# Kernel tuning notes

Hardware: AMD Instinct MI355X
Metric: run time of the kernel (lower is better)

Reference implementation:

```python
import jax, jax.numpy as jnp
import jax.lax as lax
import numpy as np

B, T, IN, H, OUT = 1024, 730, 64, 512, 1

def setup_inputs() -> dict:
    key = jax.random.key(0)
    ks = jax.random.split(key, 7)
    s_ih = 1.0 / np.sqrt(IN)
    s_hh = 1.0 / np.sqrt(H)
    return {
        "xd": jax.random.normal(ks[0], (B, T, IN), dtype=jnp.float32),
        "W_ih": jax.random.uniform(ks[1], (4 * H, IN), minval=-s_ih, maxval=s_ih, dtype=jnp.float32),
        "W_hh": jax.random.uniform(ks[2], (4 * H, H), minval=-s_hh, maxval=s_hh, dtype=jnp.float32),
        "b": jax.random.uniform(ks[3], (4 * H,), minval=-s_hh, maxval=s_hh, dtype=jnp.float32),
        "Wl": jax.random.uniform(ks[4], (OUT, H), minval=-s_hh, maxval=s_hh, dtype=jnp.float32),
        "bl": jax.random.uniform(ks[5], (OUT,), minval=-s_hh, maxval=s_hh, dtype=jnp.float32),
    }

def reference(xd, W_ih, W_hh, b, Wl, bl):
    # xd: [B, T, IN]. LSTM scan over time with batched carry [B, H].
    Bn = xd.shape[0]
    Hn = W_hh.shape[1]
    xs = jnp.swapaxes(xd, 0, 1)  # [T, B, IN]
    # Precompute input projections for all timesteps (one big GEMM).
    x_proj = jnp.einsum('tbi,gi->tbg', xs, W_ih) + b  # [T, B, 4H]

    def step(carry, xp_t):
        h, c = carry
        z = xp_t + h @ W_hh.T  # [B, 4H]
        i, f, g, o = jnp.split(z, 4, axis=-1)
        c = jax.nn.sigmoid(f) * c + jax.nn.sigmoid(i) * jnp.tanh(g)
        h = jax.nn.sigmoid(o) * jnp.tanh(c)
        return (h, c), None

    init = (jnp.zeros((Bn, Hn), xd.dtype), jnp.zeros((Bn, Hn), xd.dtype))
    (h_T, _), _ = lax.scan(step, init, x_proj)
    # Linear head + relu on final hidden state.
    return jax.nn.relu(h_T @ Wl.T + bl)  # [B, OUT]
```

## Files before the change

kernel.cpp:

```cpp
#include <hip/hip_runtime.h>
#include <hip/hip_bf16.h>

#define Bn   1024
#define Tn   730
#define INn  64
#define Hn   512
#define Kn   576
#define G4n  2048

typedef __bf16 bf16x8 __attribute__((ext_vector_type(8)));
typedef float  f32x4  __attribute__((ext_vector_type(4)));

#define ZROW   524
#define Z_OFF  36864

__global__ void convert_weights(const float* __restrict__ Wih,
                                const float* __restrict__ Whh,
                                __bf16* __restrict__ Wc) {
    int idx = blockIdx.x * 256 + threadIdx.x;
    if (idx >= G4n * Kn) return;
    int row = idx / Kn;
    int k   = idx - row * Kn;
    float v = (k < INn) ? Wih[row * INn + k] : Whh[row * Hn + (k - INn)];
    Wc[idx] = (__bf16)v;
}

__device__ __forceinline__ float sigf(float x)   { return __builtin_amdgcn_rcpf(1.0f + __expf(-x)); }
__device__ __forceinline__ float tanhf_f(float x){ return 2.0f * sigf(2.0f * x) - 1.0f; }

__global__ __launch_bounds__(512, 1) void lstm_persist(
    const float* __restrict__ xd,
    const float* __restrict__ bias,
    const __bf16* __restrict__ Wc,
    __bf16* __restrict__ h0,
    __bf16* __restrict__ h1,
    unsigned int* __restrict__ bar)
{
    __shared__ __align__(16) char smem[Z_OFF + ZROW * 32 * 4];
    bf16x8* aTile = (bf16x8*)smem;
    float*  zT    = (float*)(smem + Z_OFF);

    const int blk  = blockIdx.x;
    const int rg_i = (blk & 7) * 4 + ((blk >> 3) & 3);
    const int cb   = blk >> 5;
    const int m0   = rg_i << 5;
    const int j0   = cb << 6;

    const int tid  = threadIdx.x;
    const int wave = tid >> 6;
    const int lane = tid & 63;
    const int q    = lane >> 4;
    const int l16  = lane & 15;

    const int kh = wave & 1;
    const int cq = wave >> 1;

    bf16x8 wreg[9][4];
    float  bini[4];
    #pragma unroll
    for (int cg = 0; cg < 4; ++cg) {
        const int gcg  = cq * 4 + cg;
        const int gate = gcg >> 2;
        const int col  = j0 + (gcg & 3) * 16 + l16;
        #pragma unroll
        for (int kb = 0; kb < 9; ++kb)
            wreg[kb][cg] = *(const bf16x8*)(Wc + (size_t)(gate * Hn + col) * Kn
                                               + (kh * 9 + kb) * 32 + q * 8);
        bini[cg] = kh ? 0.f : bias[gate * Hn + col];
    }

    const int r  = tid >> 4;
    const int c4 = (tid & 15) << 2;
    float creg[4] = {0.f, 0.f, 0.f, 0.f};

    const int xt    = tid & 255;
    const int xrg   = (xt >> 7) & 1;
    const int xkb   = (xt >> 6) & 1;
    const int xlane = xt & 63;
    const int xq    = xlane >> 4;
    const int xl16  = xlane & 15;
    const float* xrb = xd + (size_t)(m0 + xrg * 16 + xl16) * (Tn * INn) + xkb * 32 + xq * 8;
    const int xslot  = (xrg * 18 + xkb) * 64 + xlane;
    const bool xown  = (tid < 256);

    unsigned int* cnt = bar + (rg_i << 5);
    bool dead = false;

    if (xown) {
        f32x4 lo = *(const f32x4*)xrb;
        f32x4 hi = *(const f32x4*)(xrb + 4);
        bf16x8 v;
        v[0] = (__bf16)lo[0]; v[1] = (__bf16)lo[1]; v[2] = (__bf16)lo[2]; v[3] = (__bf16)lo[3];
        v[4] = (__bf16)hi[0]; v[5] = (__bf16)hi[1]; v[6] = (__bf16)hi[2]; v[7] = (__bf16)hi[3];
        aTile[xslot] = v;
    }

    for (int t = 0; t < Tn; ++t) {
        const __bf16* hread  = (t & 1) ? h1 : h0;
        __bf16*       hwrite = (t & 1) ? h0 : h1;

        unsigned long long hu[4][2];
        #pragma unroll
        for (int i = 0; i < 4; ++i) {
            const int hf  = wave * 4 + i;
            const int rg  = hf >> 4;
            const int kbh = hf & 15;
            const unsigned long long* hp = (const unsigned long long*)
                (hread + (size_t)(m0 + rg * 16 + l16) * Hn + kbh * 32 + q * 8);
            hu[i][0] = __hip_atomic_load(hp,     __ATOMIC_RELAXED, __HIP_MEMORY_SCOPE_AGENT);
            hu[i][1] = __hip_atomic_load(hp + 1, __ATOMIC_RELAXED, __HIP_MEMORY_SCOPE_AGENT);
        }
        #pragma unroll
        for (int i = 0; i < 4; ++i) {
            const int hf  = wave * 4 + i;
            const int rg  = hf >> 4;
            const int kbh = hf & 15;
            union { unsigned long long u[2]; bf16x8 v; } cv;
            cv.u[0] = hu[i][0]; cv.u[1] = hu[i][1];
            aTile[(rg * 18 + kbh + 2) * 64 + lane] = cv.v;
        }
        __syncthreads();

        f32x4 acc[2][4];
        #pragma unroll
        for (int rg = 0; rg < 2; ++rg)
            #pragma unroll
            for (int cg = 0; cg < 4; ++cg)
                acc[rg][cg] = (f32x4){bini[cg], bini[cg], bini[cg], bini[cg]};
        #pragma unroll
        for (int kb = 0; kb < 9; ++kb) {
            const bf16x8 af0 = aTile[(0 * 18 + kh * 9 + kb) * 64 + lane];
            const bf16x8 af1 = aTile[(1 * 18 + kh * 9 + kb) * 64 + lane];
            #pragma unroll
            for (int cg = 0; cg < 4; ++cg) {
                acc[0][cg] = __builtin_amdgcn_mfma_f32_16x16x32_bf16(af0, wreg[kb][cg], acc[0][cg], 0, 0, 0);
                acc[1][cg] = __builtin_amdgcn_mfma_f32_16x16x32_bf16(af1, wreg[kb][cg], acc[1][cg], 0, 0, 0);
            }
        }
        #pragma unroll
        for (int rg = 0; rg < 2; ++rg)
            #pragma unroll
            for (int cg = 0; cg < 4; ++cg)
                #pragma unroll
                for (int e = 0; e < 4; ++e)
                    zT[(rg * 16 + q * 4 + e) * ZROW + kh * 256 + (cq * 4 + cg) * 16 + l16]
                        = acc[rg][cg][e];
        __syncthreads();

        f32x4 xlo, xhi;
        const bool mx = xown && (t + 1 < Tn);
        if (mx) {
            const float* xp = xrb + (size_t)(t + 1) * INn;
            xlo = *(const f32x4*)xp;
            xhi = *(const f32x4*)(xp + 4);
        }

        float zg[4][4];
        #pragma unroll
        for (int g = 0; g < 4; ++g) {
            f32x4 v0 = *(const f32x4*)&zT[r * ZROW +       g * 64 + c4];
            f32x4 v1 = *(const f32x4*)&zT[r * ZROW + 256 + g * 64 + c4];
            f32x4 s  = v0 + v1;
            zg[g][0] = s[0]; zg[g][1] = s[1]; zg[g][2] = s[2]; zg[g][3] = s[3];
        }
        union { unsigned long long u; __bf16 h[4]; } pk;
        #pragma unroll
        for (int cc = 0; cc < 4; ++cc) {
            const float cn = sigf(zg[1][cc]) * creg[cc]
                           + sigf(zg[0][cc]) * tanhf_f(zg[2][cc]);
            creg[cc] = cn;
            pk.h[cc] = (__bf16)(sigf(zg[3][cc]) * tanhf_f(cn));
        }
        __hip_atomic_store((unsigned long long*)(hwrite + (size_t)(m0 + r) * Hn + j0 + c4),
                           pk.u, __ATOMIC_RELAXED, __HIP_MEMORY_SCOPE_AGENT);

        if (mx) {
            bf16x8 v;
            v[0] = (__bf16)xlo[0]; v[1] = (__bf16)xlo[1]; v[2] = (__bf16)xlo[2]; v[3] = (__bf16)xlo[3];
            v[4] = (__bf16)xhi[0]; v[5] = (__bf16)xhi[1]; v[6] = (__bf16)xhi[2]; v[7] = (__bf16)xhi[3];
            aTile[xslot] = v;
        }

        __syncthreads();
        if (tid == 0) {
            __hip_atomic_fetch_add(cnt, 1u, __ATOMIC_RELAXED, __HIP_MEMORY_SCOPE_AGENT);
            if (!dead) {
                const unsigned int target = 8u * (unsigned int)(t + 1);
                int spins = 0;
                while (__hip_atomic_load(cnt, __ATOMIC_RELAXED, __HIP_MEMORY_SCOPE_AGENT) < target) {
                    __builtin_amdgcn_s_sleep(2);
                    if (++spins > 300000) { dead = true; break; }
                }
            }
        }
        __syncthreads();
    }
}

__global__ void head_kernel(const __bf16* __restrict__ h, const float* __restrict__ Wl,
                            const float* __restrict__ bl, float* __restrict__ out) {
    const int b = blockIdx.x;
    const int lane = threadIdx.x;
    const __bf16* hp = h + (size_t)b * Hn;
    float s = 0.f;
    #pragma unroll
    for (int j = lane; j < Hn; j += 64) s += (float)hp[j] * Wl[j];
    #pragma unroll
    for (int off = 32; off > 0; off >>= 1) s += __shfl_down(s, off, 64);
    if (lane == 0) out[b] = fmaxf(s + bl[0], 0.0f);
}

extern "C" void kernel_launch(void* const* d_in, const int* in_sizes, int n_in,
                              void* d_out, int out_size, void* d_ws, size_t ws_size,
                              hipStream_t stream) {
    const float* xd  = (const float*)d_in[0];
    const float* Wih = (const float*)d_in[1];
    const float* Whh = (const float*)d_in[2];
    const float* b   = (const float*)d_in[3];
    const float* Wl  = (const float*)d_in[4];
    const float* bl  = (const float*)d_in[5];
    float* out = (float*)d_out;

    char* ws = (char*)d_ws;
    __bf16* Wc = (__bf16*)ws;
    __bf16* h0 = (__bf16*)(ws + 2359296);
    __bf16* h1 = (__bf16*)(ws + 2359296 + 1048576);
    unsigned int* bar = (unsigned int*)(ws + 2359296 + 2 * 1048576);

    hipMemsetAsync(h0, 0, 1048576, stream);
    hipMemsetAsync(bar, 0, 4096, stream);

    const int total = G4n * Kn;
    convert_weights<<<(total + 255) / 256, 256, 0, stream>>>(Wih, Whh, Wc);

    lstm_persist<<<256, 512, 0, stream>>>(xd, b, Wc, h0, h1, bar);

    head_kernel<<<Bn, 64, 0, stream>>>(h0, Wl, bl, out);
}
```

Baseline: 3.631 ms.

## Remap MFMA columns so each wave owns all four gates for its hidden units

Weight columns are reassigned so each wave's four column groups are the i,f,g,o gates of the same 16 hidden units. The two K-halves then exchange only the other row-group's partial sums through a smaller LDS buffer, replacing the full z transpose through shared memory. The gate nonlinearity is computed directly in MFMA accumulator registers. The cost is that h is now written as 2-byte atomic stores, scattered over four rows, instead of one 8-byte store per thread.

```diff
diff --git a/kernel.cpp b/kernel.cpp
--- a/kernel.cpp
+++ b/kernel.cpp
@@ -11,8 +11,7 @@
 typedef __bf16 bf16x8 __attribute__((ext_vector_type(8)));
 typedef float  f32x4  __attribute__((ext_vector_type(4)));
 
-#define ZROW   524
-#define Z_OFF  36864
+#define XCH_OFF 36864
 
 __global__ void convert_weights(const float* __restrict__ Wih,
                                 const float* __restrict__ Whh,
@@ -36,9 +35,9 @@
     __bf16* __restrict__ h1,
     unsigned int* __restrict__ bar)
 {
-    __shared__ __align__(16) char smem[Z_OFF + ZROW * 32 * 4];
+    __shared__ __align__(16) char smem[XCH_OFF + 32768];
     bf16x8* aTile = (bf16x8*)smem;
-    float*  zT    = (float*)(smem + Z_OFF);
+    f32x4*  xch   = (f32x4*)(smem + XCH_OFF);
 
     const int blk  = blockIdx.x;
     const int rg_i = (blk & 7) * 4 + ((blk >> 3) & 3);
@@ -52,36 +51,29 @@
     const int q    = lane >> 4;
     const int l16  = lane & 15;
 
-    const int kh = wave & 1;
-    const int cq = wave >> 1;
+    const int kh   = wave & 1;
+    const int wq   = wave >> 1;
+    const int myrg = kh;
+    const int org  = 1 - kh;
 
     bf16x8 wreg[9][4];
     float  bini[4];
+    const int wcol = j0 + wq * 16 + l16;
     #pragma unroll
     for (int cg = 0; cg < 4; ++cg) {
-        const int gcg  = cq * 4 + cg;
-        const int gate = gcg >> 2;
-        const int col  = j0 + (gcg & 3) * 16 + l16;
         #pragma unroll
         for (int kb = 0; kb < 9; ++kb)
-            wreg[kb][cg] = *(const bf16x8*)(Wc + (size_t)(gate * Hn + col) * Kn
+            wreg[kb][cg] = *(const bf16x8*)(Wc + (size_t)(cg * Hn + wcol) * Kn
                                                + (kh * 9 + kb) * 32 + q * 8);
-        bini[cg] = kh ? 0.f : bias[gate * Hn + col];
+        bini[cg] = bias[cg * Hn + wcol];
     }
 
-    const int r  = tid >> 4;
-    const int c4 = (tid & 15) << 2;
     float creg[4] = {0.f, 0.f, 0.f, 0.f};
 
-    const int xt    = tid & 255;
-    const int xrg   = (xt >> 7) & 1;
-    const int xkb   = (xt >> 6) & 1;
-    const int xlane = xt & 63;
-    const int xq    = xlane >> 4;
-    const int xl16  = xlane & 15;
-    const float* xrb = xd + (size_t)(m0 + xrg * 16 + xl16) * (Tn * INn) + xkb * 32 + xq * 8;
-    const int xslot  = (xrg * 18 + xkb) * 64 + xlane;
-    const bool xown  = (tid < 256);
+    const bool  xown = (kh == 0);
+    const float* xrb = xd + (size_t)(m0 + (wq >> 1) * 16 + l16) * (Tn * INn)
+                          + (wq & 1) * 32 + q * 8;
+    const int   xslot = ((wq >> 1) * 18 + (wq & 1)) * 64 + lane;
 
     unsigned int* cnt = bar + (rg_i << 5);
     bool dead = false;
@@ -125,8 +117,10 @@
         #pragma unroll
         for (int rg = 0; rg < 2; ++rg)
             #pragma unroll
-            for (int cg = 0; cg < 4; ++cg)
-                acc[rg][cg] = (f32x4){bini[cg], bini[cg], bini[cg], bini[cg]};
+            for (int cg = 0; cg < 4; ++cg) {
+                const float bv = (rg == myrg) ? bini[cg] : 0.f;
+                acc[rg][cg] = (f32x4){bv, bv, bv, bv};
+            }
         #pragma unroll
         for (int kb = 0; kb < 9; ++kb) {
             const bf16x8 af0 = aTile[(0 * 18 + kh * 9 + kb) * 64 + lane];
@@ -138,13 +132,8 @@
             }
         }
         #pragma unroll
-        for (int rg = 0; rg < 2; ++rg)
-            #pragma unroll
-            for (int cg = 0; cg < 4; ++cg)
-                #pragma unroll
-                for (int e = 0; e < 4; ++e)
-                    zT[(rg * 16 + q * 4 + e) * ZROW + kh * 256 + (cq * 4 + cg) * 16 + l16]
-                        = acc[rg][cg][e];
+        for (int cg = 0; cg < 4; ++cg)
+            xch[((wq * 2 + org) * 4 + cg) * 64 + lane] = acc[org][cg];
         __syncthreads();
 
         f32x4 xlo, xhi;
@@ -154,25 +143,24 @@
             xlo = *(const f32x4*)xp;
             xhi = *(const f32x4*)(xp + 4);
         }
-
-        float zg[4][4];
-        #pragma unroll
-        for (int g = 0; g < 4; ++g) {
-            f32x4 v0 = *(const f32x4*)&zT[r * ZROW +       g * 64 + c4];
-            f32x4 v1 = *(const f32x4*)&zT[r * ZROW + 256 + g * 64 + c4];
-            f32x4 s  = v0 + v1;
-            zg[g][0] = s[0]; zg[g][1] = s[1]; zg[g][2] = s[2]; zg[g][3] = s[3];
-        }
-        union { unsigned long long u; __bf16 h[4]; } pk;
-        #pragma unroll
-        for (int cc = 0; cc < 4; ++cc) {
-            const float cn = sigf(zg[1][cc]) * creg[cc]
-                           + sigf(zg[0][cc]) * tanhf_f(zg[2][cc]);
-            creg[cc] = cn;
-            pk.h[cc] = (__bf16)(sigf(zg[3][cc]) * tanhf_f(cn));
-        }
-        __hip_atomic_store((unsigned long long*)(hwrite + (size_t)(m0 + r) * Hn + j0 + c4),
-                           pk.u, __ATOMIC_RELAXED, __HIP_MEMORY_SCOPE_AGENT);
+        float zs[4][4];
+        #pragma unroll
+        for (int cg = 0; cg < 4; ++cg) {
+            const f32x4 p = xch[((wq * 2 + myrg) * 4 + cg) * 64 + lane];
+            #pragma unroll
+            for (int e = 0; e < 4; ++e) zs[cg][e] = acc[myrg][cg][e] + p[e];
+        }
+        __bf16* hcb = hwrite + (size_t)(m0 + myrg * 16 + q * 4) * Hn + wcol;
+        #pragma unroll
+        for (int e = 0; e < 4; ++e) {
+            const float cn = sigf(zs[1][e]) * creg[e]
+                           + sigf(zs[0][e]) * tanhf_f(zs[2][e]);
+            creg[e] = cn;
+            union { __bf16 b; unsigned short u; } hv;
+            hv.b = (__bf16)(sigf(zs[3][e]) * tanhf_f(cn));
+            __hip_atomic_store((unsigned short*)(hcb + (size_t)e * Hn),
+                               hv.u, __ATOMIC_RELAXED, __HIP_MEMORY_SCOPE_AGENT);
+        }
 
         if (mx) {
             bf16x8 v;
```

New measurement: 10.14 ms. 2.79x slower.

## Load recurrent h fragments directly into MFMA registers, bypassing LDS staging

Applied to the files above, without the earlier changes.

Each wave now loads its own A-operand fragments of the hidden state straight from global memory into registers for the MFMAs, instead of cooperatively staging the whole h tile into shared memory and synchronizing. Only the small x slice remains in LDS, which removes one __syncthreads per timestep and shrinks the LDS footprint. In exchange, the four waves that share a K half each load the same h fragments, so global/L2 h traffic per block rises roughly fourfold. Loads are split into two row groups to limit register pressure.

```diff
diff --git a/kernel.cpp b/kernel.cpp
--- a/kernel.cpp
+++ b/kernel.cpp
@@ -12,7 +12,7 @@
 typedef float  f32x4  __attribute__((ext_vector_type(4)));
 
 #define ZROW   524
-#define Z_OFF  36864
+#define Z_OFF  4096
 
 __global__ void convert_weights(const float* __restrict__ Wih,
                                 const float* __restrict__ Whh,
@@ -37,7 +37,7 @@
     unsigned int* __restrict__ bar)
 {
     __shared__ __align__(16) char smem[Z_OFF + ZROW * 32 * 4];
-    bf16x8* aTile = (bf16x8*)smem;
+    bf16x8* xTile = (bf16x8*)smem;
     float*  zT    = (float*)(smem + Z_OFF);
 
     const int blk  = blockIdx.x;
@@ -73,6 +73,10 @@
     const int c4 = (tid & 15) << 2;
     float creg[4] = {0.f, 0.f, 0.f, 0.f};
 
+    const __bf16* hrow0 = (const __bf16*)0;
+    const size_t  hoff0 = (size_t)(m0 +      l16) * Hn + q * 8;
+    const size_t  hoff1 = (size_t)(m0 + 16 + l16) * Hn + q * 8;
+
     const int xt    = tid & 255;
     const int xrg   = (xt >> 7) & 1;
     const int xkb   = (xt >> 6) & 1;
@@ -80,7 +84,7 @@
     const int xq    = xlane >> 4;
     const int xl16  = xlane & 15;
     const float* xrb = xd + (size_t)(m0 + xrg * 16 + xl16) * (Tn * INn) + xkb * 32 + xq * 8;
-    const int xslot  = (xrg * 18 + xkb) * 64 + xlane;
+    const int xslot  = (xrg * 2 + xkb) * 64 + xlane;
     const bool xown  = (tid < 256);
 
     unsigned int* cnt = bar + (rg_i << 5);
@@ -92,51 +96,66 @@
         bf16x8 v;
         v[0] = (__bf16)lo[0]; v[1] = (__bf16)lo[1]; v[2] = (__bf16)lo[2]; v[3] = (__bf16)lo[3];
         v[4] = (__bf16)hi[0]; v[5] = (__bf16)hi[1]; v[6] = (__bf16)hi[2]; v[7] = (__bf16)hi[3];
-        aTile[xslot] = v;
+        xTile[xslot] = v;
     }
+    __syncthreads();
 
     for (int t = 0; t < Tn; ++t) {
         const __bf16* hread  = (t & 1) ? h1 : h0;
         __bf16*       hwrite = (t & 1) ? h0 : h1;
 
-        unsigned long long hu[4][2];
-        #pragma unroll
-        for (int i = 0; i < 4; ++i) {
-            const int hf  = wave * 4 + i;
-            const int rg  = hf >> 4;
-            const int kbh = hf & 15;
-            const unsigned long long* hp = (const unsigned long long*)
-                (hread + (size_t)(m0 + rg * 16 + l16) * Hn + kbh * 32 + q * 8);
-            hu[i][0] = __hip_atomic_load(hp,     __ATOMIC_RELAXED, __HIP_MEMORY_SCOPE_AGENT);
-            hu[i][1] = __hip_atomic_load(hp + 1, __ATOMIC_RELAXED, __HIP_MEMORY_SCOPE_AGENT);
-        }
-        #pragma unroll
-        for (int i = 0; i < 4; ++i) {
-            const int hf  = wave * 4 + i;
-            const int rg  = hf >> 4;
-            const int kbh = hf & 15;
-            union { unsigned long long u[2]; bf16x8 v; } cv;
-            cv.u[0] = hu[i][0]; cv.u[1] = hu[i][1];
-            aTile[(rg * 18 + kbh + 2) * 64 + lane] = cv.v;
-        }
-        __syncthreads();
-
         f32x4 acc[2][4];
         #pragma unroll
         for (int rg = 0; rg < 2; ++rg)
             #pragma unroll
             for (int cg = 0; cg < 4; ++cg)
                 acc[rg][cg] = (f32x4){bini[cg], bini[cg], bini[cg], bini[cg]};
-        #pragma unroll
-        for (int kb = 0; kb < 9; ++kb) {
-            const bf16x8 af0 = aTile[(0 * 18 + kh * 9 + kb) * 64 + lane];
-            const bf16x8 af1 = aTile[(1 * 18 + kh * 9 + kb) * 64 + lane];
-            #pragma unroll
-            for (int cg = 0; cg < 4; ++cg) {
-                acc[0][cg] = __builtin_amdgcn_mfma_f32_16x16x32_bf16(af0, wreg[kb][cg], acc[0][cg], 0, 0, 0);
-                acc[1][cg] = __builtin_amdgcn_mfma_f32_16x16x32_bf16(af1, wreg[kb][cg], acc[1][cg], 0, 0, 0);
+
+        {
+            bf16x8 a0[9];
+            #pragma unroll
+            for (int kb = 0; kb < 9; ++kb) {
+                const int kg = kh * 9 + kb;
+                if (kg < 2) {
+                    a0[kb] = xTile[(0 * 2 + kg) * 64 + lane];
+                } else {
+                    const unsigned long long* hp = (const unsigned long long*)
+                        (hread + hoff0 + (size_t)(kg - 2) * 32);
+                    union { unsigned long long u[2]; bf16x8 v; } cv;
+                    cv.u[0] = __hip_atomic_load(hp,     __ATOMIC_RELAXED, __HIP_MEMORY_SCOPE_AGENT);
+                    cv.u[1] = __hip_atomic_load(hp + 1, __ATOMIC_RELAXED, __HIP_MEMORY_SCOPE_AGENT);
+                    a0[kb] = cv.v;
+                }
             }
-        }
+            #pragma unroll
+            for (int kb = 0; kb < 9; ++kb)
+                #pragma unroll
+                for (int cg = 0; cg < 4; ++cg)
+                    acc[0][cg] = __builtin_amdgcn_mfma_f32_16x16x32_bf16(a0[kb], wreg[kb][cg], acc[0][cg], 0, 0, 0);
+        }
+        {
+            bf16x8 a1[9];
+            #pragma unroll
+            for (int kb = 0; kb < 9; ++kb) {
+                const int kg = kh * 9 + kb;
+                if (kg < 2) {
+                    a1[kb] = xTile[(1 * 2 + kg) * 64 + lane];
+                } else {
+                    const unsigned long long* hp = (const unsigned long long*)
+                        (hread + hoff1 + (size_t)(kg - 2) * 32);
+                    union { unsigned long long u[2]; bf16x8 v; } cv;
+                    cv.u[0] = __hip_atomic_load(hp,     __ATOMIC_RELAXED, __HIP_MEMORY_SCOPE_AGENT);
+                    cv.u[1] = __hip_atomic_load(hp + 1, __ATOMIC_RELAXED, __HIP_MEMORY_SCOPE_AGENT);
+                    a1[kb] = cv.v;
+                }
+            }
+            #pragma unroll
+            for (int kb = 0; kb < 9; ++kb)
+                #pragma unroll
+                for (int cg = 0; cg < 4; ++cg)
+                    acc[1][cg] = __builtin_amdgcn_mfma_f32_16x16x32_bf16(a1[kb], wreg[kb][cg], acc[1][cg], 0, 0, 0);
+        }
+
         #pragma unroll
         for (int rg = 0; rg < 2; ++rg)
             #pragma unroll
@@ -178,7 +197,7 @@
             bf16x8 v;
             v[0] = (__bf16)xlo[0]; v[1] = (__bf16)xlo[1]; v[2] = (__bf16)xlo[2]; v[3] = (__bf16)xlo[3];
             v[4] = (__bf16)xhi[0]; v[5] = (__bf16)xhi[1]; v[6] = (__bf16)xhi[2]; v[7] = (__bf16)xhi[3];
-            aTile[xslot] = v;
+            xTile[xslot] = v;
         }
 
         __syncthreads();
```

Result: slower. 6.563 ms (+80.8%).
